# Kernel optimization log

Measured on AMD Instinct MI355X. Metric: run time of the kernel, lower is better.

## Reference

```python
import jax, jax.numpy as jnp
import numpy as np

B, HD, NQ, NC, NH, NL, NP, NLAY, DFF = 8, 256, 300, 80, 8, 3, 4, 6, 1024
SHAPES = [(80, 80), (40, 40), (20, 20)]
FEAT_CH = [512, 1024, 2048]
DH = HD // NH
EPS_ANCHOR = 0.01


def _linear(x, w, b):
    return x @ w.T + b


def _ln(x, g, b):
    m = x.mean(-1, keepdims=True)
    v = ((x - m) ** 2).mean(-1, keepdims=True)
    return (x - m) / jnp.sqrt(v + 1e-5) * g + b


def _mlp3(x, w1, b1, w2, b2, w3, b3):
    x = jax.nn.relu(_linear(x, w1, b1))
    x = jax.nn.relu(_linear(x, w2, b2))
    return _linear(x, w3, b3)


def _inv_sigmoid(x, eps=1e-5):
    x = jnp.clip(x, 0.0, 1.0)
    return jnp.log(jnp.clip(x, eps, None) / jnp.clip(1.0 - x, eps, None))


def _anchors():
    parts = []
    for lvl, (h, w) in enumerate(SHAPES):
        gy, gx = jnp.meshgrid(jnp.arange(h, dtype=jnp.float32), jnp.arange(w, dtype=jnp.float32), indexing='ij')
        xy = jnp.stack([(gx + 0.5) / w, (gy + 0.5) / h], -1).reshape(-1, 2)
        wh = jnp.full_like(xy, 0.05 * (2.0 ** lvl))
        parts.append(jnp.concatenate([xy, wh], -1))
    a = jnp.concatenate(parts, 0)[None]  # [1, L, 4]
    valid = jnp.all((a > EPS_ANCHOR) & (a < 1 - EPS_ANCHOR), -1, keepdims=True)
    a = jnp.log(a / (1 - a))
    a = jnp.where(valid, a, jnp.float32(1e6))  # finite sentinel for torch's inf
    return a, valid.astype(jnp.float32)


def _mha(q_in, k_in, v_in, wqkv, bqkv, wo, bo):
    wq, wk, wv = jnp.split(wqkv, 3, 0)
    bq, bk, bv = jnp.split(bqkv, 3, 0)
    q = _linear(q_in, wq, bq)
    k = _linear(k_in, wk, bk)
    v = _linear(v_in, wv, bv)
    Bq = q.shape[0]
    sp = lambda t: t.reshape(Bq, -1, NH, DH).transpose(0, 2, 1, 3)
    q, k, v = sp(q), sp(k), sp(v)
    att = jax.nn.softmax(jnp.einsum('bhqd,bhkd->bhqk', q, k) * (1.0 / np.sqrt(DH)), -1)
    out = jnp.einsum('bhqk,bhkd->bhqd', att, v).transpose(0, 2, 1, 3).reshape(Bq, -1, HD)
    return _linear(out, wo, bo)


def _msda(value, loc, aw):
    # value [B,Len,NH,DH], loc [B,Q,NH,NL,NP,2] in [0,1], aw [B,Q,NH,NL,NP]
    Bq, Q = loc.shape[0], loc.shape[1]
    out = jnp.zeros((Bq, Q, NH, DH), value.dtype)
    start = 0
    for lvl, (h, w) in enumerate(SHAPES):
        v = value[:, start:start + h * w]  # [B,hw,NH,DH]
        start += h * w
        # grid_sample align_corners=False pixel coords
        x = loc[..., lvl, :, 0] * w - 0.5  # [B,Q,NH,NP]
        y = loc[..., lvl, :, 1] * h - 0.5
        x0 = jnp.floor(x)
        y0 = jnp.floor(y)
        lx = x - x0
        ly = y - y0
        acc = jnp.zeros((Bq, Q, NH, NP, DH), value.dtype)
        for dy, dx, wt in ((0, 0, (1 - lx) * (1 - ly)), (0, 1, lx * (1 - ly)), (1, 0, (1 - lx) * ly), (1, 1, lx * ly)):
            xi = x0 + dx
            yi = y0 + dy
            ok = ((xi >= 0) & (xi < w) & (yi >= 0) & (yi < h)).astype(value.dtype)  # zero padding
            idx = (jnp.clip(yi, 0, h - 1) * w + jnp.clip(xi, 0, w - 1)).astype(jnp.int32)
            idxf = idx.transpose(0, 1, 3, 2).reshape(Bq, Q * NP, NH)
            g = jnp.take_along_axis(v, idxf[..., None], axis=1)  # [B,Q*NP,NH,DH]
            g = g.reshape(Bq, Q, NP, NH, DH).transpose(0, 1, 3, 2, 4)
            acc = acc + g * (wt * ok)[..., None]
        out = out + (acc * aw[..., lvl, :, None]).sum(3)
    return out.reshape(Bq, Q, HD)


def reference(feat0, feat1, feat2, pw0, bg0, bb0, pw1, bg1, bb1, pw2, bg2, bb2,
              eo_w, eo_b, eln_g, eln_b, es_w, es_b,
              eb_w1, eb_b1, eb_w2, eb_b2, eb_w3, eb_b3,
              qp_w1, qp_b1, qp_w2, qp_b2,
              d_qkv_w, d_qkv_b, d_ao_w, d_ao_b, d_ln1_g, d_ln1_b,
              d_off_w, d_off_b, d_aw_w, d_aw_b, d_val_w, d_val_b,
              d_out_w, d_out_b, d_ln2_g, d_ln2_b,
              d_f1_w, d_f1_b, d_f2_w, d_f2_b, d_ln3_g, d_ln3_b,
              d_sc_w, d_sc_b, d_bb_w1, d_bb_b1, d_bb_w2, d_bb_b2, d_bb_w3, d_bb_b3):
    feats = [feat0, feat1, feat2]
    pws, bgs, bbs = [pw0, pw1, pw2], [bg0, bg1, bg2], [bb0, bb1, bb2]
    toks = []
    for f, pw, g, b in zip(feats, pws, bgs, bbs):
        # 1x1 conv (no bias) + BatchNorm eval (running mean 0, var 1 -> affine)
        t = jnp.einsum('bchw,oc->bhwo', f, pw) * g + b
        toks.append(t.reshape(f.shape[0], -1, HD))
    memory = jnp.concatenate(toks, 1)  # [B, 8400, 256]
    anchors, valid = _anchors()
    memory = memory * valid
    out_mem = _ln(_linear(memory, eo_w, eo_b), eln_g, eln_b)
    scores = _linear(out_mem, es_w, es_b)  # [B,L,NC]
    _, topi = jax.lax.top_k(scores.max(-1), NQ)  # 'default' query select
    gather = lambda t: jnp.take_along_axis(t, topi[..., None], axis=1)
    sel_mem = gather(out_mem)
    anc_b = jnp.broadcast_to(anchors, (memory.shape[0],) + anchors.shape[1:])
    ref_unact = _mlp3(sel_mem, eb_w1, eb_b1, eb_w2, eb_b2, eb_w3, eb_b3) + gather(anc_b)
    tgt = jax.lax.stop_gradient(sel_mem)
    ref = jax.nn.sigmoid(jax.lax.stop_gradient(ref_unact))  # [B,NQ,4]
    Bq = memory.shape[0]
    for i in range(NLAY):
        qpos = _linear(jax.nn.relu(_linear(ref, qp_w1, qp_b1)), qp_w2, qp_b2)
        q = tgt + qpos
        a = _mha(q, q, tgt, d_qkv_w[i], d_qkv_b[i], d_ao_w[i], d_ao_b[i])
        tgt = _ln(tgt + a, d_ln1_g[i], d_ln1_b[i])
        qc = tgt + qpos
        off = _linear(qc, d_off_w[i], d_off_b[i]).reshape(Bq, NQ, NH, NL, NP, 2)
        aw = jax.nn.softmax(_linear(qc, d_aw_w[i], d_aw_b[i]).reshape(Bq, NQ, NH, NL * NP), -1)
        aw = aw.reshape(Bq, NQ, NH, NL, NP)
        r = ref[:, :, None, None, None, :]
        loc = r[..., :2] + off / NP * r[..., 2:] * 0.5
        val = _linear(memory, d_val_w[i], d_val_b[i]).reshape(Bq, -1, NH, DH)
        ca = _linear(_msda(val, loc, aw), d_out_w[i], d_out_b[i])
        tgt = _ln(tgt + ca, d_ln2_g[i], d_ln2_b[i])
        f = _linear(jax.nn.relu(_linear(tgt, d_f1_w[i], d_f1_b[i])), d_f2_w[i], d_f2_b[i])
        tgt = _ln(tgt + f, d_ln3_g[i], d_ln3_b[i])
        delta = _mlp3(tgt, d_bb_w1[i], d_bb_b1[i], d_bb_w2[i], d_bb_b2[i], d_bb_w3[i], d_bb_b3[i])
        new_ref = jax.nn.sigmoid(delta + _inv_sigmoid(ref))
        ref = jax.lax.stop_gradient(new_ref) if i < NLAY - 1 else new_ref
    logits = _linear(tgt, d_sc_w[-1], d_sc_b[-1])
    return jnp.concatenate([logits, ref], -1)  # [B, NQ, NC+4]


def setup_inputs():
    key = jax.random.key(0)
    ks = iter(jax.random.split(key, 80))
    def rn(shape, s=0.02):
        return jax.random.normal(next(ks), shape, jnp.float32) * s
    inp = {}
    for i, (c, (h, w)) in enumerate(zip(FEAT_CH, SHAPES)):
        inp['feat%d' % i] = rn((B, c, h, w), 1.0)
        inp['pw%d' % i] = rn((HD, c), (2.0 / c) ** 0.5)
        inp['bg%d' % i] = jnp.ones((HD,), jnp.float32)
        inp['bb%d' % i] = jnp.zeros((HD,), jnp.float32)
    inp['eo_w'] = rn((HD, HD)); inp['eo_b'] = jnp.zeros((HD,), jnp.float32)
    inp['eln_g'] = jnp.ones((HD,), jnp.float32); inp['eln_b'] = jnp.zeros((HD,), jnp.float32)
    inp['es_w'] = rn((NC, HD)); inp['es_b'] = jnp.zeros((NC,), jnp.float32)
    inp['eb_w1'] = rn((HD, HD)); inp['eb_b1'] = jnp.zeros((HD,), jnp.float32)
    inp['eb_w2'] = rn((HD, HD)); inp['eb_b2'] = jnp.zeros((HD,), jnp.float32)
    inp['eb_w3'] = rn((4, HD)); inp['eb_b3'] = jnp.zeros((4,), jnp.float32)
    inp['qp_w1'] = rn((2 * HD, 4)); inp['qp_b1'] = jnp.zeros((2 * HD,), jnp.float32)
    inp['qp_w2'] = rn((HD, 2 * HD)); inp['qp_b2'] = jnp.zeros((HD,), jnp.float32)
    L = NLAY
    inp['d_qkv_w'] = rn((L, 3 * HD, HD)); inp['d_qkv_b'] = jnp.zeros((L, 3 * HD), jnp.float32)
    inp['d_ao_w'] = rn((L, HD, HD)); inp['d_ao_b'] = jnp.zeros((L, HD), jnp.float32)
    inp['d_ln1_g'] = jnp.ones((L, HD), jnp.float32); inp['d_ln1_b'] = jnp.zeros((L, HD), jnp.float32)
    inp['d_off_w'] = rn((L, NH * NL * NP * 2, HD), 0.005); inp['d_off_b'] = rn((L, NH * NL * NP * 2), 0.1)
    inp['d_aw_w'] = rn((L, NH * NL * NP, HD)); inp['d_aw_b'] = jnp.zeros((L, NH * NL * NP), jnp.float32)
    inp['d_val_w'] = rn((L, HD, HD)); inp['d_val_b'] = jnp.zeros((L, HD), jnp.float32)
    inp['d_out_w'] = rn((L, HD, HD)); inp['d_out_b'] = jnp.zeros((L, HD), jnp.float32)
    inp['d_ln2_g'] = jnp.ones((L, HD), jnp.float32); inp['d_ln2_b'] = jnp.zeros((L, HD), jnp.float32)
    inp['d_f1_w'] = rn((L, DFF, HD)); inp['d_f1_b'] = jnp.zeros((L, DFF), jnp.float32)
    inp['d_f2_w'] = rn((L, HD, DFF)); inp['d_f2_b'] = jnp.zeros((L, HD), jnp.float32)
    inp['d_ln3_g'] = jnp.ones((L, HD), jnp.float32); inp['d_ln3_b'] = jnp.zeros((L, HD), jnp.float32)
    inp['d_sc_w'] = rn((L, NC, HD)); inp['d_sc_b'] = jnp.zeros((L, NC), jnp.float32)
    inp['d_bb_w1'] = rn((L, HD, HD)); inp['d_bb_b1'] = jnp.zeros((L, HD), jnp.float32)
    inp['d_bb_w2'] = rn((L, HD, HD)); inp['d_bb_b2'] = jnp.zeros((L, HD), jnp.float32)
    inp['d_bb_w3'] = rn((L, 4, HD)); inp['d_bb_b3'] = jnp.zeros((L, 4), jnp.float32)
    return inp
```

## Files before the change

kernel.cpp:

```cpp
#include <hip/hip_runtime.h>

constexpr int Bb  = 8;
constexpr int HDn = 256;
constexpr int NQn = 300;
constexpr int NCn = 80;
constexpr int NHn = 8;
constexpr int NPn = 4;
constexpr int Sn  = 8400;
constexpr int MQ  = Bb * NQn;
constexpr int MS  = Bb * Sn;

typedef __attribute__((ext_vector_type(8))) short short8;
typedef __attribute__((ext_vector_type(4))) float floatx4;

__device__ __forceinline__ unsigned short f2bf(float f) {
    unsigned u = __float_as_uint(f);
    unsigned r = u + 0x7FFFu + ((u >> 16) & 1u);
    return (unsigned short)(r >> 16);
}
__device__ __forceinline__ unsigned pack2(float a, float b) {
    return (unsigned)f2bf(a) | ((unsigned)f2bf(b) << 16);
}

__global__ __launch_bounds__(256) void proj_kernel(
    const float* __restrict__ feat, const float* __restrict__ pw,
    const float* __restrict__ bg, const float* __restrict__ bb,
    float* __restrict__ mem,
    int C, int HW, int Wdim, int base)
{
    const int b = blockIdx.z;
    const float* Afeat = feat + (size_t)b * C * HW;
    __shared__ float As[16][128];
    __shared__ float Ws[16][64];
    const int tid = threadIdx.x;
    const int tx = tid & 15, ty = tid >> 4;
    const int p0 = blockIdx.x * 128, o0 = blockIdx.y * 64;
    const int pp4 = (tid & 31) * 4;
    const int cb = tid >> 5;
    const int wrow = tid & 63, wk = (tid >> 6) * 4;
    float acc[8][4] = {};
    for (int k0 = 0; k0 < C; k0 += 16) {
        float4 va0 = make_float4(0.f,0.f,0.f,0.f), va1 = va0;
        if (p0 + pp4 < HW) {
            va0 = *reinterpret_cast<const float4*>(Afeat + (size_t)(k0 + cb) * HW + p0 + pp4);
            va1 = *reinterpret_cast<const float4*>(Afeat + (size_t)(k0 + cb + 8) * HW + p0 + pp4);
        }
        const float4 vw = *reinterpret_cast<const float4*>(pw + (size_t)(o0 + wrow) * C + k0 + wk);
        __syncthreads();
        As[cb][pp4 + 0] = va0.x; As[cb][pp4 + 1] = va0.y; As[cb][pp4 + 2] = va0.z; As[cb][pp4 + 3] = va0.w;
        As[cb + 8][pp4 + 0] = va1.x; As[cb + 8][pp4 + 1] = va1.y; As[cb + 8][pp4 + 2] = va1.z; As[cb + 8][pp4 + 3] = va1.w;
        Ws[wk + 0][wrow] = vw.x; Ws[wk + 1][wrow] = vw.y; Ws[wk + 2][wrow] = vw.z; Ws[wk + 3][wrow] = vw.w;
        __syncthreads();
#pragma unroll
        for (int k = 0; k < 16; ++k) {
// ... 23 lines not shown
        }
    }
}

__global__ __launch_bounds__(512) void gemm_eoln(
    const float* __restrict__ A,
    const float* __restrict__ W,
    const float* __restrict__ bias,
    const float* __restrict__ g, const float* __restrict__ bt,
    float* __restrict__ O)
{
    __shared__ float As[16][128];
    __shared__ float Ws[16][256];
    const int tid = threadIdx.x;
    const int tx = tid & 31;
    const int ty = tid >> 5;
    const int m0 = blockIdx.x * 128;
    const int arow = tid >> 2, ak = (tid & 3) * 4;
    const int wrow = tid >> 1, wk = (tid & 1) * 8;
    float acc[8][8] = {};
    for (int k0 = 0; k0 < 256; k0 += 16) {
        const float4 a4 = *reinterpret_cast<const float4*>(A + (size_t)(m0 + arow) * 256 + k0 + ak);
        const float4 w0 = *reinterpret_cast<const float4*>(W + (size_t)wrow * 256 + k0 + wk);
        const float4 w1 = *reinterpret_cast<const float4*>(W + (size_t)wrow * 256 + k0 + wk + 4);
        __syncthreads();
        As[ak + 0][arow] = a4.x; As[ak + 1][arow] = a4.y; As[ak + 2][arow] = a4.z; As[ak + 3][arow] = a4.w;
        Ws[wk + 0][wrow] = w0.x; Ws[wk + 1][wrow] = w0.y; Ws[wk + 2][wrow] = w0.z; Ws[wk + 3][wrow] = w0.w;
        Ws[wk + 4][wrow] = w1.x; Ws[wk + 5][wrow] = w1.y; Ws[wk + 6][wrow] = w1.z; Ws[wk + 7][wrow] = w1.w;
        __syncthreads();
#pragma unroll
        for (int k = 0; k < 16; ++k) {
            const float4 a0 = *reinterpret_cast<const float4*>(&As[k][ty * 8]);
            const float4 a1 = *reinterpret_cast<const float4*>(&As[k][ty * 8 + 4]);
            const float4 wv0 = *reinterpret_cast<const float4*>(&Ws[k][tx * 8]);
            const float4 wv1 = *reinterpret_cast<const float4*>(&Ws[k][tx * 8 + 4]);
            const float av[8] = {a0.x, a0.y, a0.z, a0.w, a1.x, a1.y, a1.z, a1.w};
            const float wv[8] = {wv0.x, wv0.y, wv0.z, wv0.w, wv1.x, wv1.y, wv1.z, wv1.w};
#pragma unroll
            for (int i = 0; i < 8; ++i)
#pragma unroll
                for (int j = 0; j < 8; ++j)
                    acc[i][j] = fmaf(av[i], wv[j], acc[i][j]);
        }
    }
    float bv[8], gv[8], btv[8];
#pragma unroll
    for (int j = 0; j < 8; ++j) {
        bv[j] = bias[tx * 8 + j];
        gv[j] = g[tx * 8 + j];
        btv[j] = bt[tx * 8 + j];
    }
#pragma unroll
    for (int i = 0; i < 8; ++i) {
        float s1 = 0.f, s2 = 0.f;
#pragma unroll
        for (int j = 0; j < 8; ++j) {
            const float v = acc[i][j] + bv[j];
            acc[i][j] = v;
            s1 += v; s2 += v * v;
        }
#pragma unroll
        for (int o = 1; o < 32; o <<= 1) {
            s1 += __shfl_xor(s1, o, 64);
            s2 += __shfl_xor(s2, o, 64);
        }
        const float mean = s1 * (1.f / 256.f);
        const float var  = s2 * (1.f / 256.f) - mean * mean;
        const float inv  = rsqrtf(var + 1e-5f);
        float out[8];
#pragma unroll
        for (int j = 0; j < 8; ++j) out[j] = (acc[i][j] - mean) * inv * gv[j] + btv[j];
        float* op = O + (size_t)(m0 + ty * 8 + i) * 256 + tx * 8;
        *reinterpret_cast<float4*>(op) = make_float4(out[0], out[1], out[2], out[3]);
        *reinterpret_cast<float4*>(op + 4) = make_float4(out[4], out[5], out[6], out[7]);
    }
}

__global__ __launch_bounds__(256) void gemm_es(
    const float* __restrict__ A,
    const float* __restrict__ W,
    const float* __restrict__ bias,
    float* __restrict__ smax)
{
    __shared__ float As[16][64];
    __shared__ float Ws[16][80];
    const int tid = threadIdx.x;
    const int tx = tid & 15;
    const int ty = tid >> 4;
    const int m0 = blockIdx.x * 64;
    const int arow = tid >> 2, ak = (tid & 3) * 4;
    float acc[4][5] = {};
    for (int k0 = 0; k0 < 256; k0 += 16) {
        const float4 a4 = *reinterpret_cast<const float4*>(A + (size_t)(m0 + arow) * 256 + k0 + ak);
        float4 w0 = make_float4(0.f,0.f,0.f,0.f), w1 = w0;
        const int wrow = tid >> 1, wk = (tid & 1) * 8;
        if (tid < 160) {
            w0 = *reinterpret_cast<const float4*>(W + (size_t)wrow * 256 + k0 + wk);
            w1 = *reinterpret_cast<const float4*>(W + (size_t)wrow * 256 + k0 + wk + 4);
        }
        __syncthreads();
        As[ak + 0][arow] = a4.x; As[ak + 1][arow] = a4.y; As[ak + 2][arow] = a4.z; As[ak + 3][arow] = a4.w;
        if (tid < 160) {
            Ws[wk + 0][wrow] = w0.x; Ws[wk + 1][wrow] = w0.y; Ws[wk + 2][wrow] = w0.z; Ws[wk + 3][wrow] = w0.w;
            Ws[wk + 4][wrow] = w1.x; Ws[wk + 5][wrow] = w1.y; Ws[wk + 6][wrow] = w1.z; Ws[wk + 7][wrow] = w1.w;
        }
        __syncthreads();
#pragma unroll
        for (int k = 0; k < 16; ++k) {
            const float4 a4v = *reinterpret_cast<const float4*>(&As[k][ty * 4]);
            const float av[4] = {a4v.x, a4v.y, a4v.z, a4v.w};
            float wv[5];
#pragma unroll
            for (int j = 0; j < 5; ++j) wv[j] = Ws[k][tx * 5 + j];
#pragma unroll
            for (int i = 0; i < 4; ++i)
#pragma unroll
                for (int j = 0; j < 5; ++j)
                    acc[i][j] = fmaf(av[i], wv[j], acc[i][j]);
        }
    }
    float bv[5];
#pragma unroll
    for (int j = 0; j < 5; ++j) bv[j] = bias[tx * 5 + j];
#pragma unroll
    for (int i = 0; i < 4; ++i) {
        float vmax = -3.0e38f;
#pragma unroll
        for (int j = 0; j < 5; ++j) vmax = fmaxf(vmax, acc[i][j] + bv[j]);
#pragma unroll
        for (int o = 1; o < 16; o <<= 1) vmax = fmaxf(vmax, __shfl_xor(vmax, o, 64));
        if (tx == 0) smax[m0 + ty * 4 + i] = vmax;
    }
}

__global__ void fconv_kernel(const float* __restrict__ in, unsigned short* __restrict__ out, int n4)
{
    const int i = blockIdx.x * 256 + threadIdx.x;
    if (i >= n4) return;
    const float4 v = reinterpret_cast<const float4*>(in)[i];
    reinterpret_cast<uint2*>(out)[i] = make_uint2(pack2(v.x, v.y), pack2(v.z, v.w));
}

__global__ __launch_bounds__(512) void gemm_vbig(
    const unsigned short* __restrict__ A,
    const float* __restrict__ W,
    const float* __restrict__ bias,
    unsigned short* __restrict__ C,
    int M)
{
    __shared__ __align__(16) unsigned short As[128 * 40];
    __shared__ __align__(16) unsigned short Bs[256 * 40];
    const int tid = threadIdx.x;
    const int lane = tid & 63, wid = tid >> 6;
    const int wm = wid >> 2, wn = wid & 3;
    const int m0 = blockIdx.x * 128, n0 = blockIdx.y * 256;
    const int arow = tid >> 2, ak = (tid & 3) * 8;
    const int brow = tid >> 1, bk = (tid & 1) * 16;
    const int fs = (lane >> 4) * 8;
    floatx4 acc[4][4];
#pragma unroll
    for (int i = 0; i < 4; ++i)
#pragma unroll
        for (int j = 0; j < 4; ++j) acc[i][j] = (floatx4){0.f, 0.f, 0.f, 0.f};

    for (int k0 = 0; k0 < 256; k0 += 32) {
        const short8 a8 = *reinterpret_cast<const short8*>(A + (size_t)(m0 + arow) * 256 + k0 + ak);
        float wv[16];
        {
            const float* wp = W + (size_t)(n0 + brow) * 256 + k0 + bk;
#pragma unroll
            for (int j = 0; j < 4; ++j) *reinterpret_cast<float4*>(&wv[4 * j]) = *reinterpret_cast<const float4*>(wp + 4 * j);
        }
        __syncthreads();
        *reinterpret_cast<short8*>(&As[arow * 40 + ak]) = a8;
        *reinterpret_cast<uint4*>(&Bs[brow * 40 + bk]) =
            make_uint4(pack2(wv[0], wv[1]), pack2(wv[2], wv[3]), pack2(wv[4], wv[5]), pack2(wv[6], wv[7]));
        *reinterpret_cast<uint4*>(&Bs[brow * 40 + bk + 8]) =
            make_uint4(pack2(wv[8], wv[9]), pack2(wv[10], wv[11]), pack2(wv[12], wv[13]), pack2(wv[14], wv[15]));
        __syncthreads();
        short8 af[4], bf[4];
#pragma unroll
        for (int mi = 0; mi < 4; ++mi)
            af[mi] = *reinterpret_cast<const short8*>(&As[(wm * 64 + mi * 16 + (lane & 15)) * 40 + fs]);
#pragma unroll
        for (int ni = 0; ni < 4; ++ni)
            bf[ni] = *reinterpret_cast<const short8*>(&Bs[(wn * 64 + ni * 16 + (lane & 15)) * 40 + fs]);
#pragma unroll
        for (int mi = 0; mi < 4; ++mi)
#pragma unroll
            for (int ni = 0; ni < 4; ++ni)
                acc[mi][ni] = __builtin_amdgcn_mfma_f32_16x16x32_bf16(af[mi], bf[ni], acc[mi][ni], 0, 0, 0);
    }
#pragma unroll
    for (int mi = 0; mi < 4; ++mi) {
        const int rowb = m0 + wm * 64 + mi * 16 + (lane >> 4) * 4;
#pragma unroll
        for (int ni = 0; ni < 4; ++ni) {
            const int col = n0 + wn * 64 + ni * 16 + (lane & 15);
            const float bv = bias[col];
#pragma unroll
            for (int r = 0; r < 4; ++r)
                C[(size_t)(rowb + r) * 1536 + col] = f2bf(acc[mi][ni][r] + bv);
        }
    }
}

template <int ACT>
__global__ __launch_bounds__(256) void gemm_sm(
    const float* __restrict__ A, const float* __restrict__ A2, int a2_nlim, int lda,
    const float* __restrict__ W, int ldw,
    const float* __restrict__ bias,
    float* __restrict__ C, int ldc,
    int M, int N, int K)
{
    constexpr int LD = 264;
    __shared__ __align__(16) unsigned short As[64 * LD];
    __shared__ __align__(16) unsigned short Bs[64 * LD];
    const int tid = threadIdx.x;
    const int lane = tid & 63, wid = tid >> 6;
    const int wr = wid >> 1, wc = wid & 1;
    const int m0 = blockIdx.x * 64, n0 = blockIdx.y * 64;
    const float* A2e = (A2 && n0 < a2_nlim) ? A2 : nullptr;
    const int srow = tid >> 2;
    const int cb   = (tid & 3) * 16;
    const int fs = (lane >> 4) * 8;
    floatx4 acc[2][2];
#pragma unroll
    for (int i = 0; i < 2; ++i)
#pragma unroll
        for (int j = 0; j < 2; ++j) acc[i][j] = (floatx4){0.f, 0.f, 0.f, 0.f};

    for (int kc = 0; kc < K; kc += 256) {
        if (kc) __syncthreads();
        {
            const bool mok = (m0 + srow < M);
// ... 39 lines not shown
        __syncthreads();
#pragma unroll
        for (int ks = 0; ks < 8; ++ks) {
            short8 af[2], bf[2];
#pragma unroll
            for (int mi = 0; mi < 2; ++mi)
                af[mi] = *reinterpret_cast<const short8*>(&As[(wr * 32 + mi * 16 + (lane & 15)) * LD + ks * 32 + fs]);
#pragma unroll
            for (int ni = 0; ni < 2; ++ni)
                bf[ni] = *reinterpret_cast<const short8*>(&Bs[(wc * 32 + ni * 16 + (lane & 15)) * LD + ks * 32 + fs]);
#pragma unroll
            for (int mi = 0; mi < 2; ++mi)
#pragma unroll
                for (int ni = 0; ni < 2; ++ni)
                    acc[mi][ni] = __builtin_amdgcn_mfma_f32_16x16x32_bf16(af[mi], bf[ni], acc[mi][ni], 0, 0, 0);
        }
    }
#pragma unroll
    for (int mi = 0; mi < 2; ++mi) {
        const int rowb = m0 + wr * 32 + mi * 16 + (lane >> 4) * 4;
#pragma unroll
        for (int ni = 0; ni < 2; ++ni) {
            const int col = n0 + wc * 32 + ni * 16 + (lane & 15);
            if (col >= N) continue;
            const float bv = bias[col];
#pragma unroll
            for (int r = 0; r < 4; ++r) {
                const int row = rowb + r;
                if (row >= M) continue;
                float v = acc[mi][ni][r] + bv;
                if (ACT == 1) v = fmaxf(v, 0.f);
                C[(size_t)row * ldc + col] = v;
            }
        }
    }
}

__global__ __launch_bounds__(256) void gemm_qpos(
    const float* __restrict__ ref, const float* __restrict__ w1, const float* __restrict__ b1,
    const float* __restrict__ W2, const float* __restrict__ b2,
    float* __restrict__ C, int M)
{
    __shared__ __align__(16) unsigned short As_h[128 * 40];
    __shared__ __align__(16) unsigned short Bs_h[128 * 40];
    __shared__ float w1s[512 * 4];
    __shared__ float b1s[512];
    const int tid = threadIdx.x;
    const int lane = tid & 63, wid = tid >> 6;
    const int wm = wid >> 1, wn = wid & 1;
    const int m0 = blockIdx.x * 128, n0 = blockIdx.y * 128;
    const int srow = tid >> 1, skoff = (tid & 1) * 16;
    const int fs = (lane >> 4) * 8;
    for (int i = tid; i < 512 * 4; i += 256) w1s[i] = w1[i];
    for (int i = tid; i < 512; i += 256) b1s[i] = b1[i];
    float rv0 = 0.f, rv1 = 0.f, rv2 = 0.f, rv3 = 0.f;
    if (m0 + srow < M) {
        const float* rp = ref + (size_t)(m0 + srow) * 4;
        rv0 = rp[0]; rv1 = rp[1]; rv2 = rp[2]; rv3 = rp[3];
    }
    floatx4 acc[4][4];
#pragma unroll
    for (int i = 0; i < 4; ++i)
#pragma unroll
        for (int j = 0; j < 4; ++j) acc[i][j] = (floatx4){0.f, 0.f, 0.f, 0.f};
    __syncthreads();

// ... 25 lines not shown
#pragma unroll
        for (int mi = 0; mi < 4; ++mi) {
            const int r = wm * 64 + mi * 16 + (lane & 15);
            af[mi] = *reinterpret_cast<const short8*>(&As_h[r * 40 + fs]);
        }
#pragma unroll
        for (int ni = 0; ni < 4; ++ni) {
            const int r = wn * 64 + ni * 16 + (lane & 15);
            bff[ni] = *reinterpret_cast<const short8*>(&Bs_h[r * 40 + fs]);
        }
#pragma unroll
        for (int mi = 0; mi < 4; ++mi)
#pragma unroll
            for (int ni = 0; ni < 4; ++ni)
                acc[mi][ni] = __builtin_amdgcn_mfma_f32_16x16x32_bf16(af[mi], bff[ni], acc[mi][ni], 0, 0, 0);
    }
#pragma unroll
    for (int mi = 0; mi < 4; ++mi) {
        const int rowb = m0 + wm * 64 + mi * 16 + (lane >> 4) * 4;
#pragma unroll
        for (int ni = 0; ni < 4; ++ni) {
            const int col = n0 + wn * 64 + ni * 16 + (lane & 15);
            const float bv = b2[col];
#pragma unroll
            for (int r = 0; r < 4; ++r) {
                const int row = rowb + r;
                if (row >= M) continue;
                C[(size_t)row * HDn + col] = acc[mi][ni][r] + bv;
            }
        }
    }
}

__global__ __launch_bounds__(256) void ln_kernel(
    const float* __restrict__ X, const float* __restrict__ R,
    const float* __restrict__ g, const float* __restrict__ bta,
    float* __restrict__ O)
{
    const int m = blockIdx.x;
    const int t = threadIdx.x;
    float v = X[(size_t)m * HDn + t] + R[(size_t)m * HDn + t];
    float s1 = v, s2 = v * v;
#pragma unroll
    for (int o = 32; o > 0; o >>= 1) {
        s1 += __shfl_down(s1, o, 64);
        s2 += __shfl_down(s2, o, 64);
    }
    __shared__ float a1[4], a2[4];
    if ((t & 63) == 0) { a1[t >> 6] = s1; a2[t >> 6] = s2; }
    __syncthreads();
    const float S1 = a1[0] + a1[1] + a1[2] + a1[3];
    const float S2 = a2[0] + a2[1] + a2[2] + a2[3];
    const float mean = S1 * (1.f / HDn);
    const float var  = S2 * (1.f / HDn) - mean * mean;
    const float inv  = rsqrtf(var + 1e-5f);
    O[(size_t)m * HDn + t] = (v - mean) * inv * g[t] + bta[t];
}

__global__ __launch_bounds__(256) void topk_kernel(const float* __restrict__ smax, int* __restrict__ topi)
{
    const int b = blockIdx.x, t = threadIdx.x;
    __shared__ float vals[Sn];
    __shared__ int hist[256];
    __shared__ unsigned long long sel[NQn];
    __shared__ unsigned long long s_prefix;
    __shared__ int s_need;
    __shared__ int s_cnt;
    for (int i = t; i < Sn; i += 256) vals[i] = smax[(size_t)b * Sn + i];
    if (t == 0) { s_prefix = 0ULL; s_need = NQn; s_cnt = 0; }
    __syncthreads();

    for (int shift = 56; shift >= 0; shift -= 8) {
        if (t < 256) hist[t] = 0;
        __syncthreads();
        const unsigned long long prefix = s_prefix;
        const unsigned long long mask = (shift == 56) ? 0ULL : (~0ULL << (shift + 8));
        for (int i = t; i < Sn; i += 256) {
            unsigned uk = __float_as_uint(vals[i]);
            uk = (uk & 0x80000000u) ? ~uk : (uk | 0x80000000u);
            const unsigned long long key = ((unsigned long long)uk << 32) | (unsigned)(Sn - i);
            if ((key & mask) == prefix)
                atomicAdd(&hist[(int)((key >> shift) & 255)], 1);
        }
        __syncthreads();
        if (t == 0) {
            int need = s_need, accum = 0, v = 255;
            for (; v >= 0; --v) {
                const int c = hist[v];
                if (accum + c >= need) break;
                accum += c;
            }
// ... 144 lines not shown
            for (int d = 0; d < 32; ++d) Om[q][d] = o[d];
        }
    }
    __syncthreads();
    if (!half && q < NQn) {
        const float m2 = Mm[q], l2 = Lm[q];
        const float mm = fmaxf(m, m2);
        const float c1 = __expf(m - mm), c2 = __expf(m2 - mm);
        const float L = l * c1 + l2 * c2;
        const float inv = 1.f / L;
        float* op = O + ((size_t)(b * NQn + q)) * HDn + h * 32;
#pragma unroll
        for (int d = 0; d < 32; ++d) op[d] = (o[d] * c1 + Om[q][d] * c2) * inv;
    }
}

__global__ void concat_oaw(const float* __restrict__ offw, const float* __restrict__ offbias,
                           const float* __restrict__ aww, const float* __restrict__ awbias,
                           float* __restrict__ cw, float* __restrict__ cb)
{
    const int idx = blockIdx.x * 256 + threadIdx.x;
    const int TW = 6 * 288 * 256;
    if (idx < TW) {
        const int i = idx / (288 * 256);
        const int r = (idx / 256) % 288;
        const int c = idx & 255;
        cw[idx] = (r < 192) ? offw[((size_t)i * 192 + r) * 256 + c]
                            : aww[((size_t)i * 96 + (r - 192)) * 256 + c];
    } else if (idx < TW + 6 * 288) {
        const int j = idx - TW;
        const int i = j / 288, r = j % 288;
        cb[j] = (r < 192) ? offbias[i * 192 + r] : awbias[i * 96 + (r - 192)];
    }
}

__global__ void softmax12_kernel(float* __restrict__ oaw)
{
    const int g = blockIdx.x * 256 + threadIdx.x;
    if (g >= MQ * NHn) return;
    float* p = oaw + (size_t)(g >> 3) * 288 + 192 + (g & 7) * 12;
    float mx = -1e30f;
#pragma unroll
    for (int i = 0; i < 12; ++i) mx = fmaxf(mx, p[i]);
    float e[12];
    float s = 0.f;
#pragma unroll
    for (int i = 0; i < 12; ++i) { e[i] = expf(p[i] - mx); s += e[i]; }
    const float inv = 1.f / s;
#pragma unroll
    for (int i = 0; i < 12; ++i) p[i] = e[i] * inv;
}

__global__ __launch_bounds__(256) void msda_kernel(const unsigned short* __restrict__ val, int ldv,
                                                   const float* __restrict__ oaw,
                                                   const float* __restrict__ ref,
                                                   float* __restrict__ out)
{
    const int mq = blockIdx.x;
    const int b = mq / NQn;
    const int t = threadIdx.x;
    const int h = t >> 5, d = t & 31;
    __shared__ float s_ref[4];
    __shared__ float s_aw[96];
    __shared__ float s_off[192];
    if (t < 4) s_ref[t] = ref[mq * 4 + t];
    if (t < 96) s_aw[t] = oaw[(size_t)mq * 288 + 192 + t];
    if (t < 192) s_off[t] = oaw[(size_t)mq * 288 + t];
    __syncthreads();
    const int Wl[3] = {80, 40, 20};
    const int base[3] = {0, 6400, 8000};
    float acc = 0.f;
#pragma unroll
    for (int l = 0; l < 3; ++l) {
        const int W = Wl[l];
        const unsigned short* vb = val + ((size_t)b * Sn + base[l]) * ldv + h * 32 + d;
#pragma unroll
        for (int p = 0; p < 4; ++p) {
            const float ox = s_off[((h * 3 + l) * 4 + p) * 2 + 0];
            const float oy = s_off[((h * 3 + l) * 4 + p) * 2 + 1];
            const float locx = s_ref[0] + ox * (1.f / NPn) * s_ref[2] * 0.5f;
            const float locy = s_ref[1] + oy * (1.f / NPn) * s_ref[3] * 0.5f;
            const float x = locx * W - 0.5f;
            const float y = locy * W - 0.5f;
// ... 73 lines not shown
    const float* d_val_w = (const float*)d_in[38];
    const float* d_val_b = (const float*)d_in[39];
    const float* d_out_w = (const float*)d_in[40];
    const float* d_out_b = (const float*)d_in[41];
    const float* d_ln2_g = (const float*)d_in[42];
    const float* d_ln2_b = (const float*)d_in[43];
    const float* d_f1_w  = (const float*)d_in[44];
    const float* d_f1_b  = (const float*)d_in[45];
    const float* d_f2_w  = (const float*)d_in[46];
    const float* d_f2_b  = (const float*)d_in[47];
    const float* d_ln3_g = (const float*)d_in[48];
    const float* d_ln3_b = (const float*)d_in[49];
    const float* d_sc_w  = (const float*)d_in[50];
    const float* d_sc_b  = (const float*)d_in[51];
    const float* d_bb_w1 = (const float*)d_in[52];
    const float* d_bb_b1 = (const float*)d_in[53];
    const float* d_bb_w2 = (const float*)d_in[54];
    const float* d_bb_b2 = (const float*)d_in[55];
    const float* d_bb_w3 = (const float*)d_in[56];
    const float* d_bb_b3 = (const float*)d_in[57];

    float* ws = (float*)d_ws;
    size_t off = 0;
    auto alloc = [&](size_t n) { float* p = ws + off; off += (n + 63) & ~(size_t)63; return p; };
    float* memory = alloc((size_t)MS * HDn);
    float* om     = alloc((size_t)MS * HDn);
    float* smaxb  = alloc((size_t)MS);
    int*   topi   = (int*)alloc((size_t)MQ);
    float* tgt    = alloc((size_t)MQ * HDn);
    float* refb   = alloc((size_t)MQ * 4);
    float* qpos   = alloc((size_t)MQ * HDn);
    float* qkvb   = alloc((size_t)MQ * 768);
    float* atto   = alloc((size_t)MQ * HDn);
    float* abuf   = alloc((size_t)MQ * HDn);
    float* oawb   = alloc((size_t)MQ * 288);
    float* msd    = alloc((size_t)MQ * HDn);
    float* ffb    = alloc((size_t)MQ * 1024);
    float* qb     = alloc((size_t)MQ * HDn);
    float* kb     = alloc((size_t)MQ * HDn);
    float* cw     = alloc((size_t)6 * 288 * 256);
    float* cb     = alloc((size_t)6 * 288);
    const size_t VALBIG_FLOATS = (size_t)MS * 768;
    unsigned short* valbig = nullptr;
    if ((off + VALBIG_FLOATS + 64) * sizeof(float) <= ws_size)
        valbig = (unsigned short*)alloc(VALBIG_FLOATS);
    const bool batched = (valbig != nullptr);
    unsigned short* ombf = (unsigned short*)om;
    float* outp = (float*)d_out;

    concat_oaw<<<(6 * 288 * 256 + 6 * 288 + 255) / 256, 256, 0, stream>>>(d_off_w, d_off_b, d_aw_w, d_aw_b, cw, cb);

    proj_kernel<<<dim3(50, 4, 8), 256, 0, stream>>>(feat0, pw0, bg0, bb0, memory, 512, 6400, 80, 0);
    proj_kernel<<<dim3(13, 4, 8), 256, 0, stream>>>(feat1, pw1, bg1, bb1, memory, 1024, 1600, 40, 6400);
    proj_kernel<<<dim3(4, 4, 8), 256, 0, stream>>>(feat2, pw2, bg2, bb2, memory, 2048, 400, 20, 8000);

    gemm_eoln<<<525, 512, 0, stream>>>(memory, eo_w, eo_b, eln_g, eln_b, om);
    gemm_es<<<1050, 256, 0, stream>>>(om, es_w, es_b, smaxb);
    topk_kernel<<<Bb, 256, 0, stream>>>(smaxb, topi);
    gather_kernel<<<MQ, 256, 0, stream>>>(om, topi, tgt);

    gemm_sm<1><<<dim3(38, 4), 256, 0, stream>>>(tgt, nullptr, 0, HDn, eb_w1, HDn, eb_b1, qb, HDn, MQ, HDn, HDn);
    gemm_sm<1><<<dim3(38, 4), 256, 0, stream>>>(qb, nullptr, 0, HDn, eb_w2, HDn, eb_b2, kb, HDn, MQ, HDn, HDn);
    head4_kernel<0><<<600, 256, 0, stream>>>(kb, eb_w3, eb_b3, topi, refb);

    if (batched) {
        fconv_kernel<<<(MS * HDn / 4 + 255) / 256, 256, 0, stream>>>(memory, ombf, MS * HDn / 4);
        gemm_vbig<<<dim3(525, 6), 512, 0, stream>>>(ombf, d_val_w, d_val_b, valbig, MS);
    }

    for (int i = 0; i < 6; ++i) {
        const float* wqkv = d_qkv_w + (size_t)i * 768 * 256;
        const float* bqkv = d_qkv_b + (size_t)i * 768;
        gemm_qpos<<<dim3(19, 2), 256, 0, stream>>>(refb, qp_w1, qp_b1, qp_w2, qp_b2, qpos, MQ);
        gemm_sm<0><<<dim3(38, 12), 256, 0, stream>>>(tgt, qpos, 512, HDn, wqkv, HDn, bqkv, qkvb, 768, MQ, 768, HDn);
        mha_kernel<<<dim3(NHn, Bb), 640, 0, stream>>>(qkvb, atto);
        gemm_sm<0><<<dim3(38, 4), 256, 0, stream>>>(atto, nullptr, 0, HDn, d_ao_w + (size_t)i * 65536, HDn,
                                                    d_ao_b + (size_t)i * 256, abuf, HDn, MQ, HDn, HDn);
        ln_kernel<<<MQ, 256, 0, stream>>>(abuf, tgt, d_ln1_g + (size_t)i * 256, d_ln1_b + (size_t)i * 256, tgt);
        gemm_sm<0><<<dim3(38, 5), 256, 0, stream>>>(tgt, qpos, 1 << 30, HDn, cw + (size_t)i * 288 * 256, HDn,
                                                    cb + (size_t)i * 288, oawb, 288, MQ, 288, HDn);
        softmax12_kernel<<<(MQ * NHn + 255) / 256, 256, 0, stream>>>(oawb);
        const unsigned short* valptr;
        int ldv;
        if (batched) { valptr = valbig + (size_t)i * 256; ldv = 1536; }
        else {
            fconv_kernel<<<(MS * HDn / 4 + 255) / 256, 256, 0, stream>>>(memory, (unsigned short*)ffb, MS * HDn / 4);
            gemm_vbig<<<dim3(525, 1), 512, 0, stream>>>((unsigned short*)ffb, d_val_w + (size_t)i * 65536,
                                                        d_val_b + (size_t)i * 256, ombf, MS);
            valptr = ombf; ldv = 1536;
        }
        msda_kernel<<<MQ, 256, 0, stream>>>(valptr, ldv, oawb, refb, msd);
        gemm_sm<0><<<dim3(38, 4), 256, 0, stream>>>(msd, nullptr, 0, HDn, d_out_w + (size_t)i * 65536, HDn,
                                                    d_out_b + (size_t)i * 256, abuf, HDn, MQ, HDn, HDn);
        ln_kernel<<<MQ, 256, 0, stream>>>(abuf, tgt, d_ln2_g + (size_t)i * 256, d_ln2_b + (size_t)i * 256, tgt);
        gemm_sm<1><<<dim3(38, 16), 256, 0, stream>>>(tgt, nullptr, 0, HDn, d_f1_w + (size_t)i * 1024 * 256, HDn,
                                                     d_f1_b + (size_t)i * 1024, ffb, 1024, MQ, 1024, HDn);
        gemm_sm<0><<<dim3(38, 4), 256, 0, stream>>>(ffb, nullptr, 0, 1024, d_f2_w + (size_t)i * 256 * 1024, 1024,
                                                    d_f2_b + (size_t)i * 256, abuf, HDn, MQ, HDn, 1024);
        ln_kernel<<<MQ, 256, 0, stream>>>(abuf, tgt, d_ln3_g + (size_t)i * 256, d_ln3_b + (size_t)i * 256, tgt);
        gemm_sm<1><<<dim3(38, 4), 256, 0, stream>>>(tgt, nullptr, 0, HDn, d_bb_w1 + (size_t)i * 65536, HDn,
                                                    d_bb_b1 + (size_t)i * 256, qb, HDn, MQ, HDn, HDn);
        gemm_sm<1><<<dim3(38, 4), 256, 0, stream>>>(qb, nullptr, 0, HDn, d_bb_w2 + (size_t)i * 65536, HDn,
                                                    d_bb_b2 + (size_t)i * 256, kb, HDn, MQ, HDn, HDn);
        head4_kernel<1><<<600, 256, 0, stream>>>(kb, d_bb_w3 + (size_t)i * 1024, d_bb_b3 + (size_t)i * 4, nullptr, refb);
    }

    gemm_sm<0><<<dim3(38, 2), 256, 0, stream>>>(tgt, nullptr, 0, HDn, d_sc_w + (size_t)5 * 80 * 256, HDn,
                                                d_sc_b + (size_t)5 * 80, outp, 84, MQ, NCn, HDn);
    copy_ref_kernel<<<(MQ + 255) / 256, 256, 0, stream>>>(refb, outp);
}
```

Before: 2.587 ms.

## Fuse LayerNorm and softmax into MFMA GEMMs, drop bf16 conversion pass

```diff
diff --git a/kernel.cpp b/kernel.cpp
--- a/kernel.cpp
+++ b/kernel.cpp
@@ -20,6 +20,65 @@
 }
 __device__ __forceinline__ unsigned pack2(float a, float b) {
     return (unsigned)f2bf(a) | ((unsigned)f2bf(b) << 16);
+}
+
+__global__ __launch_bounds__(512) void proj2_kernel(
+    const float* __restrict__ feat, const float* __restrict__ pw,
+    const float* __restrict__ bg, const float* __restrict__ bb,
+    float* __restrict__ mem,
+    int C, int HW, int Wdim, int base)
+{
+    const int b = blockIdx.z;
+    const float* Af = feat + (size_t)b * C * HW;
+    __shared__ float As[16][128];
+    __shared__ float Ws[16][256];
+    const int tid = threadIdx.x;
+    const int tx = tid & 31;
+    const int ty = tid >> 5;
+    const int p0 = blockIdx.x * 128;
+    const int lc = tid >> 5, lp4 = (tid & 31) * 4;
+    const int wrow = tid >> 1, wk = (tid & 1) * 8;
+    float acc[8][8] = {};
+    for (int k0 = 0; k0 < C; k0 += 16) {
+        float4 va = make_float4(0.f, 0.f, 0.f, 0.f);
+        if (p0 + lp4 < HW) va = *reinterpret_cast<const float4*>(Af + (size_t)(k0 + lc) * HW + p0 + lp4);
+        const float4 w0 = *reinterpret_cast<const float4*>(pw + (size_t)wrow * C + k0 + wk);
+        const float4 w1 = *reinterpret_cast<const float4*>(pw + (size_t)wrow * C + k0 + wk + 4);
+        __syncthreads();
+        As[lc][lp4 + 0] = va.x; As[lc][lp4 + 1] = va.y; As[lc][lp4 + 2] = va.z; As[lc][lp4 + 3] = va.w;
+        Ws[wk + 0][wrow] = w0.x; Ws[wk + 1][wrow] = w0.y; Ws[wk + 2][wrow] = w0.z; Ws[wk + 3][wrow] = w0.w;
+        Ws[wk + 4][wrow] = w1.x; Ws[wk + 5][wrow] = w1.y; Ws[wk + 6][wrow] = w1.z; Ws[wk + 7][wrow] = w1.w;
+        __syncthreads();
+#pragma unroll
+        for (int k = 0; k < 16; ++k) {
+            const float4 a0 = *reinterpret_cast<const float4*>(&As[k][ty * 8]);
+            const float4 a1 = *reinterpret_cast<const float4*>(&As[k][ty * 8 + 4]);
+            const float av[8] = {a0.x, a0.y, a0.z, a0.w, a1.x, a1.y, a1.z, a1.w};
+            float wv[8];
+#pragma unroll
+            for (int j = 0; j < 8; ++j) wv[j] = Ws[k][tx + j * 32];
+#pragma unroll
+            for (int i = 0; i < 8; ++i)
+#pragma unroll
+                for (int j = 0; j < 8; ++j)
+                    acc[i][j] = fmaf(av[i], wv[j], acc[i][j]);
+        }
+    }
+    float bgv[8], bbv[8];
+#pragma unroll
+    for (int j = 0; j < 8; ++j) { bgv[j] = bg[tx + j * 32]; bbv[j] = bb[tx + j * 32]; }
+#pragma unroll
+    for (int i = 0; i < 8; ++i) {
+        const int pp = p0 + ty * 8 + i;
+        if (pp >= HW) continue;
+        const int yy = pp / Wdim, xx = pp - yy * Wdim;
+        const float ax = (xx + 0.5f) / Wdim, ay = (yy + 0.5f) / Wdim;
+        const float vm = ((ax > 0.01f) && (ax < 0.99f) && (ay > 0.01f) && (ay < 0.99f)) ? 1.f : 0.f;
+        float* op = mem + ((size_t)b * Sn + base + pp) * HDn;
+#pragma unroll
+        for (int j = 0; j < 8; ++j)
+            op[tx + j * 32] = (acc[i][j] * bgv[j] + bbv[j]) * vm;
+    }
 }
 
 __global__ __launch_bounds__(256) void proj_kernel(
@@ -109,10 +168,10 @@
         for (int k = 0; k < 16; ++k) {
             const float4 a0 = *reinterpret_cast<const float4*>(&As[k][ty * 8]);
             const float4 a1 = *reinterpret_cast<const float4*>(&As[k][ty * 8 + 4]);
-            const float4 wv0 = *reinterpret_cast<const float4*>(&Ws[k][tx * 8]);
-            const float4 wv1 = *reinterpret_cast<const float4*>(&Ws[k][tx * 8 + 4]);
             const float av[8] = {a0.x, a0.y, a0.z, a0.w, a1.x, a1.y, a1.z, a1.w};
-            const float wv[8] = {wv0.x, wv0.y, wv0.z, wv0.w, wv1.x, wv1.y, wv1.z, wv1.w};
+            float wv[8];
+#pragma unroll
+            for (int j = 0; j < 8; ++j) wv[j] = Ws[k][tx + j * 32];
 #pragma unroll
             for (int i = 0; i < 8; ++i)
 #pragma unroll
@@ -123,9 +182,9 @@
     float bv[8], gv[8], btv[8];
 #pragma unroll
     for (int j = 0; j < 8; ++j) {
-        bv[j] = bias[tx * 8 + j];
-        gv[j] = g[tx * 8 + j];
-        btv[j] = bt[tx * 8 + j];
+        bv[j] = bias[tx + j * 32];
+        gv[j] = g[tx + j * 32];
+        btv[j] = bt[tx + j * 32];
     }
 #pragma unroll
     for (int i = 0; i < 8; ++i) {
@@ -144,12 +203,9 @@
         const float mean = s1 * (1.f / 256.f);
         const float var  = s2 * (1.f / 256.f) - mean * mean;
         const float inv  = rsqrtf(var + 1e-5f);
-        float out[8];
-#pragma unroll
-        for (int j = 0; j < 8; ++j) out[j] = (acc[i][j] - mean) * inv * gv[j] + btv[j];
-        float* op = O + (size_t)(m0 + ty * 8 + i) * 256 + tx * 8;
-        *reinterpret_cast<float4*>(op) = make_float4(out[0], out[1], out[2], out[3]);
-        *reinterpret_cast<float4*>(op + 4) = make_float4(out[4], out[5], out[6], out[7]);
+        float* op = O + (size_t)(m0 + ty * 8 + i) * 256;
+#pragma unroll
+        for (int j = 0; j < 8; ++j) op[tx + j * 32] = (acc[i][j] - mean) * inv * gv[j] + btv[j];
     }
 }
 
@@ -210,19 +266,11 @@
     }
 }
 
-__global__ void fconv_kernel(const float* __restrict__ in, unsigned short* __restrict__ out, int n4)
-{
-    const int i = blockIdx.x * 256 + threadIdx.x;
-    if (i >= n4) return;
-    const float4 v = reinterpret_cast<const float4*>(in)[i];
-    reinterpret_cast<uint2*>(out)[i] = make_uint2(pack2(v.x, v.y), pack2(v.z, v.w));
-}
-
 __global__ __launch_bounds__(512) void gemm_vbig(
-    const unsigned short* __restrict__ A,
+    const float* __restrict__ A,
     const float* __restrict__ W,
     const float* __restrict__ bias,
-    unsigned short* __restrict__ C,
+    unsigned short* __restrict__ C, int ldc,
     int M)
 {
     __shared__ __align__(16) unsigned short As[128 * 40];
@@ -241,7 +289,12 @@
         for (int j = 0; j < 4; ++j) acc[i][j] = (floatx4){0.f, 0.f, 0.f, 0.f};
 
     for (int k0 = 0; k0 < 256; k0 += 32) {
-        const short8 a8 = *reinterpret_cast<const short8*>(A + (size_t)(m0 + arow) * 256 + k0 + ak);
+        float av[8];
+        {
+            const float* ap = A + (size_t)(m0 + arow) * 256 + k0 + ak;
+            *reinterpret_cast<float4*>(&av[0]) = *reinterpret_cast<const float4*>(ap);
+            *reinterpret_cast<float4*>(&av[4]) = *reinterpret_cast<const float4*>(ap + 4);
+        }
         float wv[16];
         {
             const float* wp = W + (size_t)(n0 + brow) * 256 + k0 + bk;
@@ -249,7 +302,8 @@
             for (int j = 0; j < 4; ++j) *reinterpret_cast<float4*>(&wv[4 * j]) = *reinterpret_cast<const float4*>(wp + 4 * j);
         }
         __syncthreads();
-        *reinterpret_cast<short8*>(&As[arow * 40 + ak]) = a8;
+        *reinterpret_cast<uint4*>(&As[arow * 40 + ak]) =
+            make_uint4(pack2(av[0], av[1]), pack2(av[2], av[3]), pack2(av[4], av[5]), pack2(av[6], av[7]));
         *reinterpret_cast<uint4*>(&Bs[brow * 40 + bk]) =
             make_uint4(pack2(wv[0], wv[1]), pack2(wv[2], wv[3]), pack2(wv[4], wv[5]), pack2(wv[6], wv[7]));
         *reinterpret_cast<uint4*>(&Bs[brow * 40 + bk + 8]) =
@@ -277,7 +331,7 @@
             const float bv = bias[col];
 #pragma unroll
             for (int r = 0; r < 4; ++r)
-                C[(size_t)(rowb + r) * 1536 + col] = f2bf(acc[mi][ni][r] + bv);
+                C[(size_t)(rowb + r) * ldc + col] = f2bf(acc[mi][ni][r] + bv);
         }
     }
 }
@@ -383,6 +437,179 @@
                 if (ACT == 1) v = fmaxf(v, 0.f);
                 C[(size_t)row * ldc + col] = v;
             }
+        }
+    }
+}
+
+template <int MODE>
+__global__ __launch_bounds__(256) void gemm_smN(
+    const float* __restrict__ A, const float* __restrict__ A2, int lda,
+    const float* __restrict__ W, int ldw,
+    const float* __restrict__ bias,
+    const float* __restrict__ R, const float* __restrict__ g, const float* __restrict__ bt,
+    float* __restrict__ C, int ldc,
+    int M, int N, int K)
+{
+    constexpr int LDH = 72;
+    __shared__ __align__(16) unsigned short As[64 * LDH];
+    __shared__ __align__(16) unsigned short Bs[288 * LDH];
+    __shared__ float red[640];
+    const int tid = threadIdx.x;
+    const int lane = tid & 63, wid = tid >> 6;
+    const int m0 = blockIdx.x * 64;
+    const int NT = N >> 4;
+    const int srow = tid >> 2, sc = (tid & 3) * 16;
+    const int fs = (lane >> 4) * 8;
+    floatx4 acc[4][5];
+#pragma unroll
+    for (int i = 0; i < 4; ++i)
+#pragma unroll
+        for (int j = 0; j < 5; ++j) acc[i][j] = (floatx4){0.f, 0.f, 0.f, 0.f};
+
+    for (int kc = 0; kc < K; kc += 64) {
+        if (kc) __syncthreads();
+        {
+            const bool mok = (m0 + srow < M);
+            const float* ap = A + (size_t)(m0 + srow) * lda + kc + sc;
+            const float* ap2 = A2 ? A2 + (size_t)(m0 + srow) * lda + kc + sc : nullptr;
+            float v[16];
+#pragma unroll
+            for (int j = 0; j < 16; ++j) v[j] = 0.f;
+            if (mok) {
+#pragma unroll
+                for (int j = 0; j < 4; ++j)
+                    *reinterpret_cast<float4*>(&v[4 * j]) = *reinterpret_cast<const float4*>(ap + 4 * j);
+                if (ap2) {
+#pragma unroll
+                    for (int j = 0; j < 16; ++j) v[j] += ap2[j];
+                }
+            }
+            *reinterpret_cast<uint4*>(&As[srow * LDH + sc]) =
+                make_uint4(pack2(v[0], v[1]), pack2(v[2], v[3]), pack2(v[4], v[5]), pack2(v[6], v[7]));
+            *reinterpret_cast<uint4*>(&As[srow * LDH + sc + 8]) =
+                make_uint4(pack2(v[8], v[9]), pack2(v[10], v[11]), pack2(v[12], v[13]), pack2(v[14], v[15]));
+        }
+        for (int r = tid; r < N; r += 256) {
+            const float* wp = W + (size_t)r * ldw + kc;
+#pragma unroll
+            for (int j = 0; j < 16; ++j) {
+                const float4 v = *reinterpret_cast<const float4*>(wp + j * 4);
+                *reinterpret_cast<uint2*>(&Bs[r * LDH + j * 4]) = make_uint2(pack2(v.x, v.y), pack2(v.z, v.w));
+            }
+        }
+        __syncthreads();
+#pragma unroll
+        for (int ks = 0; ks < 2; ++ks) {
+            short8 af[4];
+#pragma unroll
+            for (int mi = 0; mi < 4; ++mi)
+                af[mi] = *reinterpret_cast<const short8*>(&As[(mi * 16 + (lane & 15)) * LDH + ks * 32 + fs]);
+#pragma unroll
+            for (int ti = 0; ti < 5; ++ti) {
+                const int t = wid + ti * 4;
+                if (t >= NT) break;
+                const short8 bf = *reinterpret_cast<const short8*>(&Bs[(t * 16 + (lane & 15)) * LDH + ks * 32 + fs]);
+#pragma unroll
+                for (int mi = 0; mi < 4; ++mi)
+                    acc[mi][ti] = __builtin_amdgcn_mfma_f32_16x16x32_bf16(af[mi], bf, acc[mi][ti], 0, 0, 0);
+            }
+        }
+    }
+    __syncthreads();
+    if (MODE == 2) {
+#pragma unroll
+        for (int mi = 0; mi < 4; ++mi) {
+#pragma unroll
+            for (int r = 0; r < 4; ++r) {
+                const int rl = mi * 16 + (lane >> 4) * 4 + r;
+                const int row = m0 + rl;
+                float s1 = 0.f, s2 = 0.f;
+                if (row < M) {
+#pragma unroll
+                    for (int ti = 0; ti < 5; ++ti) {
+                        const int t = wid + ti * 4;
+                        if (t >= NT) break;
+                        const int col = t * 16 + (lane & 15);
+                        const float v = acc[mi][ti][r] + bias[col] + R[(size_t)row * ldc + col];
+                        s1 += v; s2 += v * v;
+                    }
+                }
+#pragma unroll
+                for (int o = 1; o < 16; o <<= 1) {
+                    s1 += __shfl_xor(s1, o, 64);
+                    s2 += __shfl_xor(s2, o, 64);
+                }
+                if ((lane & 15) == 0) {
+                    red[wid * 64 + rl] = s1;
+                    red[256 + wid * 64 + rl] = s2;
+                }
+            }
+        }
+        __syncthreads();
+        if (tid < 64) {
+            const float S1 = red[tid] + red[64 + tid] + red[128 + tid] + red[192 + tid];
+            const float S2 = red[256 + tid] + red[320 + tid] + red[384 + tid] + red[448 + tid];
+            const float mean = S1 * (1.f / 256.f);
+            const float var  = S2 * (1.f / 256.f) - mean * mean;
+            red[512 + tid] = mean;
+            red[576 + tid] = rsqrtf(var + 1e-5f);
+        }
+        __syncthreads();
+#pragma unroll
+        for (int mi = 0; mi < 4; ++mi) {
+#pragma unroll
+            for (int r = 0; r < 4; ++r) {
+                const int rl = mi * 16 + (lane >> 4) * 4 + r;
+                const int row = m0 + rl;
+                if (row >= M) continue;
+                const float mean = red[512 + rl], inv = red[576 + rl];
+#pragma unroll
+                for (int ti = 0; ti < 5; ++ti) {
+                    const int t = wid + ti * 4;
+                    if (t >= NT) break;
+                    const int col = t * 16 + (lane & 15);
+                    const float v = acc[mi][ti][r] + bias[col] + R[(size_t)row * ldc + col];
+                    C[(size_t)row * ldc + col] = (v - mean) * inv * g[col] + bt[col];
+                }
+            }
+        }
+    } else {
+        float* smb = reinterpret_cast<float*>(Bs);
+#pragma unroll
+        for (int mi = 0; mi < 4; ++mi) {
+#pragma unroll
+            for (int r = 0; r < 4; ++r) {
+                const int rl = mi * 16 + (lane >> 4) * 4 + r;
+                const int row = m0 + rl;
+                if (row >= M) continue;
+#pragma unroll
+                for (int ti = 0; ti < 5; ++ti) {
+                    const int t = wid + ti * 4;
+                    if (t >= NT) break;
+                    const int col = t * 16 + (lane & 15);
+                    const float v = acc[mi][ti][r] + bias[col];
+                    if (col < 192) C[(size_t)row * ldc + col] = v;
+                    else smb[rl * 96 + col - 192] = v;
+                }
+            }
+        }
+        __syncthreads();
+        for (int idx = tid; idx < 512; idx += 256) {
+            const int rl = idx >> 3, h = idx & 7;
+            const int row = m0 + rl;
+            if (row >= M) continue;
+            float* p = smb + rl * 96 + h * 12;
+            float mx = -1e30f;
+#pragma unroll
+            for (int i = 0; i < 12; ++i) mx = fmaxf(mx, p[i]);
+            float e[12];
+            float s = 0.f;
+#pragma unroll
+            for (int i = 0; i < 12; ++i) { e[i] = expf(p[i] - mx); s += e[i]; }
+            const float inv = 1.f / s;
+            float* cp = C + (size_t)row * ldc + 192 + h * 12;
+#pragma unroll
+            for (int i = 0; i < 12; ++i) cp[i] = e[i] * inv;
         }
     }
 }
@@ -474,31 +701,6 @@
     }
 }
 
-__global__ __launch_bounds__(256) void ln_kernel(
-    const float* __restrict__ X, const float* __restrict__ R,
-    const float* __restrict__ g, const float* __restrict__ bta,
-    float* __restrict__ O)
-{
-    const int m = blockIdx.x;
-    const int t = threadIdx.x;
-    float v = X[(size_t)m * HDn + t] + R[(size_t)m * HDn + t];
-    float s1 = v, s2 = v * v;
-#pragma unroll
-    for (int o = 32; o > 0; o >>= 1) {
-        s1 += __shfl_down(s1, o, 64);
-        s2 += __shfl_down(s2, o, 64);
-    }
-    __shared__ float a1[4], a2[4];
-    if ((t & 63) == 0) { a1[t >> 6] = s1; a2[t >> 6] = s2; }
-    __syncthreads();
-    const float S1 = a1[0] + a1[1] + a1[2] + a1[3];
-    const float S2 = a2[0] + a2[1] + a2[2] + a2[3];
-    const float mean = S1 * (1.f / HDn);
-    const float var  = S2 * (1.f / HDn) - mean * mean;
-    const float inv  = rsqrtf(var + 1e-5f);
-    O[(size_t)m * HDn + t] = (v - mean) * inv * g[t] + bta[t];
-}
-
 __global__ __launch_bounds__(256) void topk_kernel(const float* __restrict__ smax, int* __restrict__ topi)
 {
     const int b = blockIdx.x, t = threadIdx.x;
@@ -709,23 +911,6 @@
         const int i = j / 288, r = j % 288;
         cb[j] = (r < 192) ? offbias[i * 192 + r] : awbias[i * 96 + (r - 192)];
     }
-}
-
-__global__ void softmax12_kernel(float* __restrict__ oaw)
-{
-    const int g = blockIdx.x * 256 + threadIdx.x;
-    if (g >= MQ * NHn) return;
-    float* p = oaw + (size_t)(g >> 3) * 288 + 192 + (g & 7) * 12;
-    float mx = -1e30f;
-#pragma unroll
-    for (int i = 0; i < 12; ++i) mx = fmaxf(mx, p[i]);
-    float e[12];
-    float s = 0.f;
-#pragma unroll
-    for (int i = 0; i < 12; ++i) { e[i] = expf(p[i] - mx); s += e[i]; }
-    const float inv = 1.f / s;
-#pragma unroll
-    for (int i = 0; i < 12; ++i) p[i] = e[i] * inv;
 }
 
 __global__ __launch_bounds__(256) void msda_kernel(const unsigned short* __restrict__ val, int ldv,
@@ -865,7 +1050,6 @@
     float* qpos   = alloc((size_t)MQ * HDn);
     float* qkvb   = alloc((size_t)MQ * 768);
     float* atto   = alloc((size_t)MQ * HDn);
-    float* abuf   = alloc((size_t)MQ * HDn);
     float* oawb   = alloc((size_t)MQ * 288);
     float* msd    = alloc((size_t)MQ * HDn);
     float* ffb    = alloc((size_t)MQ * 1024);
@@ -883,7 +1067,7 @@
 
     concat_oaw<<<(6 * 288 * 256 + 6 * 288 + 255) / 256, 256, 0, stream>>>(d_off_w, d_off_b, d_aw_w, d_aw_b, cw, cb);
 
-    proj_kernel<<<dim3(50, 4, 8), 256, 0, stream>>>(feat0, pw0, bg0, bb0, memory, 512, 6400, 80, 0);
+    proj2_kernel<<<dim3(50, 1, 8), 512, 0, stream>>>(feat0, pw0, bg0, bb0, memory, 512, 6400, 80, 0);
     proj_kernel<<<dim3(13, 4, 8), 256, 0, stream>>>(feat1, pw1, bg1, bb1, memory, 1024, 1600, 40, 6400);
     proj_kernel<<<dim3(4, 4, 8), 256, 0, stream>>>(feat2, pw2, bg2, bb2, memory, 2048, 400, 20, 8000);
 
@@ -896,10 +1080,8 @@
     gemm_sm<1><<<dim3(38, 4), 256, 0, stream>>>(qb, nullptr, 0, HDn, eb_w2, HDn, eb_b2, kb, HDn, MQ, HDn, HDn);
     head4_kernel<0><<<600, 256, 0, stream>>>(kb, eb_w3, eb_b3, topi, refb);
 
-    if (batched) {
-        fconv_kernel<<<(MS * HDn / 4 + 255) / 256, 256, 0, stream>>>(memory, ombf, MS * HDn / 4);
-        gemm_vbig<<<dim3(525, 6), 512, 0, stream>>>(ombf, d_val_w, d_val_b, valbig, MS);
-    }
+    if (batched)
+        gemm_vbig<<<dim3(525, 6), 512, 0, stream>>>(memory, d_val_w, d_val_b, valbig, 1536, MS);
 
     for (int i = 0; i < 6; ++i) {
         const float* wqkv = d_qkv_w + (size_t)i * 768 * 256;
@@ -907,30 +1089,29 @@
         gemm_qpos<<<dim3(19, 2), 256, 0, stream>>>(refb, qp_w1, qp_b1, qp_w2, qp_b2, qpos, MQ);
         gemm_sm<0><<<dim3(38, 12), 256, 0, stream>>>(tgt, qpos, 512, HDn, wqkv, HDn, bqkv, qkvb, 768, MQ, 768, HDn);
         mha_kernel<<<dim3(NHn, Bb), 640, 0, stream>>>(qkvb, atto);
-        gemm_sm<0><<<dim3(38, 4), 256, 0, stream>>>(atto, nullptr, 0, HDn, d_ao_w + (size_t)i * 65536, HDn,
-                                                    d_ao_b + (size_t)i * 256, abuf, HDn, MQ, HDn, HDn);
-        ln_kernel<<<MQ, 256, 0, stream>>>(abuf, tgt, d_ln1_g + (size_t)i * 256, d_ln1_b + (size_t)i * 256, tgt);
-        gemm_sm<0><<<dim3(38, 5), 256, 0, stream>>>(tgt, qpos, 1 << 30, HDn, cw + (size_t)i * 288 * 256, HDn,
-                                                    cb + (size_t)i * 288, oawb, 288, MQ, 288, HDn);
-        softmax12_kernel<<<(MQ * NHn + 255) / 256, 256, 0, stream>>>(oawb);
+        gemm_smN<2><<<38, 256, 0, stream>>>(atto, nullptr, HDn, d_ao_w + (size_t)i * 65536, HDn,
+                                            d_ao_b + (size_t)i * 256, tgt, d_ln1_g + (size_t)i * 256,
+                                            d_ln1_b + (size_t)i * 256, tgt, HDn, MQ, HDn, HDn);
+        gemm_smN<3><<<38, 256, 0, stream>>>(tgt, qpos, HDn, cw + (size_t)i * 288 * 256, HDn,
+                                            cb + (size_t)i * 288, nullptr, nullptr, nullptr,
+                                            oawb, 288, MQ, 288, HDn);
         const unsigned short* valptr;
         int ldv;
         if (batched) { valptr = valbig + (size_t)i * 256; ldv = 1536; }
         else {
-            fconv_kernel<<<(MS * HDn / 4 + 255) / 256, 256, 0, stream>>>(memory, (unsigned short*)ffb, MS * HDn / 4);
-            gemm_vbig<<<dim3(525, 1), 512, 0, stream>>>((unsigned short*)ffb, d_val_w + (size_t)i * 65536,
-                                                        d_val_b + (size_t)i * 256, ombf, MS);
-            valptr = ombf; ldv = 1536;
+            gemm_vbig<<<dim3(525, 1), 512, 0, stream>>>(memory, d_val_w + (size_t)i * 65536,
+                                                        d_val_b + (size_t)i * 256, ombf, 256, MS);
+            valptr = ombf; ldv = 256;
         }
         msda_kernel<<<MQ, 256, 0, stream>>>(valptr, ldv, oawb, refb, msd);
-        gemm_sm<0><<<dim3(38, 4), 256, 0, stream>>>(msd, nullptr, 0, HDn, d_out_w + (size_t)i * 65536, HDn,
-                                                    d_out_b + (size_t)i * 256, abuf, HDn, MQ, HDn, HDn);
-        ln_kernel<<<MQ, 256, 0, stream>>>(abuf, tgt, d_ln2_g + (size_t)i * 256, d_ln2_b + (size_t)i * 256, tgt);
+        gemm_smN<2><<<38, 256, 0, stream>>>(msd, nullptr, HDn, d_out_w + (size_t)i * 65536, HDn,
+                                            d_out_b + (size_t)i * 256, tgt, d_ln2_g + (size_t)i * 256,
+                                            d_ln2_b + (size_t)i * 256, tgt, HDn, MQ, HDn, HDn);
         gemm_sm<1><<<dim3(38, 16), 256, 0, stream>>>(tgt, nullptr, 0, HDn, d_f1_w + (size_t)i * 1024 * 256, HDn,
                                                      d_f1_b + (size_t)i * 1024, ffb, 1024, MQ, 1024, HDn);
-        gemm_sm<0><<<dim3(38, 4), 256, 0, stream>>>(ffb, nullptr, 0, 1024, d_f2_w + (size_t)i * 256 * 1024, 1024,
-                                                    d_f2_b + (size_t)i * 256, abuf, HDn, MQ, HDn, 1024);
-        ln_kernel<<<MQ, 256, 0, stream>>>(abuf, tgt, d_ln3_g + (size_t)i * 256, d_ln3_b + (size_t)i * 256, tgt);
+        gemm_smN<2><<<38, 256, 0, stream>>>(ffb, nullptr, 1024, d_f2_w + (size_t)i * 256 * 1024, 1024,
+                                            d_f2_b + (size_t)i * 256, tgt, d_ln3_g + (size_t)i * 256,
+                                            d_ln3_b + (size_t)i * 256, tgt, HDn, MQ, HDn, 1024);
         gemm_sm<1><<<dim3(38, 4), 256, 0, stream>>>(tgt, nullptr, 0, HDn, d_bb_w1 + (size_t)i * 65536, HDn,
                                                     d_bb_b1 + (size_t)i * 256, qb, HDn, MQ, HDn, HDn);
         gemm_sm<1><<<dim3(38, 4), 256, 0, stream>>>(qb, nullptr, 0, HDn, d_bb_w2 + (size_t)i * 65536, HDn,
```

After: 3.658 ms. 1.41x slower.
